# Optimization experiments

Measured on AMD Instinct MI355X. Metric: run time of the kernel, lower is better.

The kernel has to match this reference:

```python
import jax, jax.numpy as jnp
import numpy as np

N = 100000          # query / support points
H = 32              # neighbors per point
CIN = 32
COUT = 64
K = 15              # kernel points
KP_EXTENT = 1.0
KERNEL_RADIUS = KP_EXTENT * 1.5


def setup_inputs() -> dict:
    key = jax.random.key(0)
    k1, k2, k3, k4, k5, k6 = jax.random.split(key, 6)
    query = jax.random.uniform(k1, (N, 3), dtype=jnp.float32)
    support = jax.random.uniform(k2, (N, 3), dtype=jnp.float32)
    edge_indices = jax.random.randint(k3, (N, H), 0, N, dtype=jnp.int32)
    features = jax.random.normal(k4, (N, CIN), dtype=jnp.float32)
    # kernel point positions within kernel radius (fixed, non-trainable)
    K_points = jax.random.normal(k5, (K, 3), dtype=jnp.float32) * (KERNEL_RADIUS / 3.0)
    K_points = K_points.at[0].set(0.0)  # fixed='center'
    # xavier-normal kernel weights [K, CIN, COUT]
    std = jnp.sqrt(2.0 / (CIN + COUT)).astype(jnp.float32)
    K_values = jax.random.normal(k6, (K, CIN, COUT), dtype=jnp.float32) * std
    return {"query": query, "support": support, "edge_indices": edge_indices,
            "features": features, "K_points": K_points, "K_values": K_values}


def reference(query, support, edge_indices, features, K_points, K_values):
    # shadow point / shadow feature for out-of-range indices
    shadow_pt = jnp.ones_like(support[:1]) * 1e6
    support_ext = jnp.concatenate([support, shadow_pt], axis=0)      # [N+1, 3]
    feats_ext = jnp.concatenate([features, jnp.zeros_like(features[:1])], axis=0)  # [N+1, CIN]

    neighbors = support_ext[edge_indices] - query[:, None, :]        # [N, H, 3]
    # squared distances to each kernel point: [N, H, K]
    diff = neighbors[:, :, None, :] - K_points[None, None, :, :]     # [N, H, K, 3]
    sq_distances = jnp.sum(diff * diff, axis=-1)                     # [N, H, K]

    # linear influence, transposed to [N, K, H]
    all_weights = jnp.maximum(1.0 - jnp.sqrt(sq_distances) / KP_EXTENT, 0.0)
    all_weights = jnp.swapaxes(all_weights, 1, 2)                    # [N, K, H]

    # aggregation_mode == 'sum': no masking
    neighborhood_features = feats_ext[edge_indices]                  # [N, H, CIN]
    weighted = jnp.einsum('nkh,nhc->nkc', all_weights, neighborhood_features)  # [N, K, CIN]
    # per-kernel-point matmul then sum over kernel points
    out = jnp.einsum('nkc,kco->no', weighted, K_values)              # [N, COUT]
    return out
```

## Files before the change

### kernel.cpp

```cpp
#include <hip/hip_runtime.h>
#include <hip/hip_bf16.h>

typedef __attribute__((ext_vector_type(8))) short short8;
typedef __attribute__((ext_vector_type(4))) float f32x4;
typedef __attribute__((ext_vector_type(2))) unsigned int u32x2;

#define HH    32
#define CINN  32
#define COUTT 64
#define KNUM  15

static __device__ __forceinline__ short bfbits(float f) {
    __hip_bfloat16 h = __float2bfloat16(f);
    short s; __builtin_memcpy(&s, &h, 2); return s;
}
static __device__ __forceinline__ unsigned packbf(float a, float b) {
    return (unsigned)(unsigned short)bfbits(a) | ((unsigned)(unsigned short)bfbits(b) << 16);
}

static __device__ __forceinline__ void lds_barrier() {
    asm volatile("s_waitcnt lgkmcnt(0)" ::: "memory");
    __builtin_amdgcn_s_barrier();
    __builtin_amdgcn_sched_barrier(0);
}

__global__ void cvt_feats_kernel(const float* __restrict__ f,
                                 unsigned short* __restrict__ o, int n8) {
    int i = blockIdx.x * blockDim.x + threadIdx.x;
    if (i < n8) {
        f32x4 v0 = *(const f32x4*)(f + i * 8);
        f32x4 v1 = *(const f32x4*)(f + i * 8 + 4);
        u32x2 s0 = { packbf(v0.x, v0.y), packbf(v0.z, v0.w) };
        u32x2 s1 = { packbf(v1.x, v1.y), packbf(v1.z, v1.w) };
        *(u32x2*)(o + i * 8)     = s0;
        *(u32x2*)(o + i * 8 + 4) = s1;
    }
}

__launch_bounds__(256, 4)
__global__ void kpconv_kernel(const float* __restrict__ query,
                              const float* __restrict__ support,
                              const int*   __restrict__ edge,
                              const unsigned short* __restrict__ featsbf,
                              const float* __restrict__ kpts,
                              const float* __restrict__ kvals,
                              float* __restrict__ out,
                              int nPts, int nBatch) {
    __shared__ unsigned short af_lds[KNUM * 64 * 8];
    __shared__ f32x4 xyz[4][4][32];

    const int tid  = threadIdx.x;
    const int wave = tid >> 6;
    const int lane = tid & 63;
    const int g    = lane >> 4;
    const int low  = lane & 15;
    const int jpar = lane >> 5;
    const int l32  = lane & 31;
    const int slotA = ((l32 & 7) << 2) | (l32 >> 3);

    short8 kvreg[KNUM];
    #pragma unroll
    for (int s = 0; s < KNUM; ++s) {
        #pragma unroll
        for (int i = 0; i < 8; ++i) {
            int cp   = (g << 3) + i;
            int chan = (((cp & 15) << 1) | (cp >> 4));
            int o    = (wave << 4) + low;
            kvreg[s][i] = bfbits(kvals[(s * CINN + chan) * COUTT + o]);
        }
    }

    float px = 1e4f, py = 1e4f, pz = 1e4f;
    if (low < KNUM) { px = kpts[low * 3 + 0]; py = kpts[low * 3 + 1]; pz = kpts[low * 3 + 2]; }

    const int  ld0  = (wave << 2) + ((g >> 1) << 4);
    const int  half = (g & 1) << 3;
    const int  dM   = (low & 7) << 4;
    const int  T0   = (low * 64 + ld0) * 16 + half;
    const int  T1   = T0 + 32 * 16;
    const bool sact = (low < KNUM);
    const unsigned lbase = (unsigned)lane << 4;

    int   eN[2]; float sxN[2], syN[2], szN[2], qxN[2], qyN[2], qzN[2];
    #define LOADA(bb)                                                          \
        _Pragma("unroll")                                                      \
        for (int k = 0; k < 2; ++k) {                                          \
            int n = (bb) * 16 + (wave << 2) + (k << 1) + jpar;                 \
            if (n >= nPts) n = nPts - 1;                                       \
            int e = edge[n * HH + l32];                                        \
            eN[k] = e;                                                         \
            const float* qp = query + n * 3;                                   \
            const float* sp = support + (size_t)(unsigned)e * 3;               \
            sxN[k] = sp[0]; syN[k] = sp[1]; szN[k] = sp[2];                    \
            qxN[k] = qp[0]; qyN[k] = qp[1]; qzN[k] = qp[2];                    \
        }

    LOADA(blockIdx.x);

    __syncthreads();

    for (int b = blockIdx.x; b < nBatch; b += gridDim.x) {
        #pragma unroll
        for (int k = 0; k < 2; ++k) {
            f32x4 v = { sxN[k] - qxN[k], syN[k] - qyN[k], szN[k] - qzN[k],
                        __int_as_float(eN[k]) };
            xyz[wave][(k << 1) + jpar][slotA] = v;
        }

        LOADA(b + gridDim.x);

        #pragma unroll
        for (int p = 0; p < 4; ++p) {
            const f32x4* xrow = &xyz[wave][p][g];

            unsigned fd[8];
            short8 wf;
            #pragma unroll
            for (int i = 0; i < 8; ++i) {
                f32x4 v = xrow[i << 2];
                unsigned e = (unsigned)__float_as_int(v.w);
                fd[i] = *(const unsigned*)((const char*)featsbf + (e << 6) + ((unsigned)low << 2));
                float tx = v.x - px, ty = v.y - py, tz = v.z - pz;
                float d2 = fmaf(tx, tx, fmaf(ty, ty, tz * tz));
                wf[i] = bfbits(fmaxf(1.f - __builtin_amdgcn_sqrtf(d2), 0.f));
            }

            short8 a0, a1;
            #pragma unroll
            for (int i = 0; i < 8; ++i) {
                a0[i] = (short)(fd[i] & 0xffffu);
                a1[i] = (short)(fd[i] >> 16);
            }

            f32x4 c0 = {0.f, 0.f, 0.f, 0.f}, c1 = {0.f, 0.f, 0.f, 0.f};
            c0 = __builtin_amdgcn_mfma_f32_16x16x32_bf16(a0, wf, c0, 0, 0, 0);
            c1 = __builtin_amdgcn_mfma_f32_16x16x32_bf16(a1, wf, c1, 0, 0, 0);

            if (sact) {
                u32x2 w0 = { packbf(c0.x, c0.y), packbf(c0.z, c0.w) };
                u32x2 w1 = { packbf(c1.x, c1.y), packbf(c1.z, c1.w) };
                *(u32x2*)((char*)af_lds + ((T0 + (p << 4)) ^ dM)) = w0;
                *(u32x2*)((char*)af_lds + ((T1 + (p << 4)) ^ dM)) = w1;
            }
        }
        lds_barrier();

        f32x4 acc = {0.f, 0.f, 0.f, 0.f};
        #pragma unroll
        for (int s = 0; s < KNUM; ++s) {
            const char* ap = (const char*)af_lds + (lbase ^ (unsigned)((s & 7) << 4)) + s * 1024;
            short8 av = *(const short8*)ap;
            acc = __builtin_amdgcn_mfma_f32_16x16x32_bf16(av, kvreg[s], acc, 0, 0, 0);
        }

        {
            int n0 = b * 16 + (g << 2);
            float* orow = out + (size_t)(unsigned)n0 * COUTT + (wave << 4) + low;
            #pragma unroll
            for (int r = 0; r < 4; ++r) {
                if (n0 + r < nPts) orow[r * COUTT] = acc[r];
            }
        }
        lds_barrier();
    }
    #undef LOADA
}

extern "C" void kernel_launch(void* const* d_in, const int* in_sizes, int n_in,
                              void* d_out, int out_size, void* d_ws, size_t ws_size,
                              hipStream_t stream) {
    const float* query   = (const float*)d_in[0];
    const float* support = (const float*)d_in[1];
    const int*   edge    = (const int*)d_in[2];
    const float* feats   = (const float*)d_in[3];
    const float* kpts    = (const float*)d_in[4];
    const float* kvals   = (const float*)d_in[5];
    float* out = (float*)d_out;

    int nPts   = in_sizes[0] / 3;
    int nBatch = (nPts + 15) / 16;

    unsigned short* featsbf = (unsigned short*)d_ws;
    int n8 = nPts * CINN / 8;
    hipLaunchKernelGGL(cvt_feats_kernel, dim3((n8 + 255) / 256), dim3(256), 0, stream,
                       feats, featsbf, n8);

    int grid = 1536;
    if (grid > nBatch) grid = nBatch;

    hipLaunchKernelGGL(kpconv_kernel, dim3(grid), dim3(256), 0, stream,
                       query, support, edge, featsbf, kpts, kvals, out, nPts, nBatch);
}
```

Measured before the change: 161.6 us.

## Batch feature gathers across two rows and precompute squared norms

Edge indices move into a separate LDS array. Feature gathers for two neighbor rows are now issued together, before the weight computation, to raise memory-level parallelism. The squared distance is expanded as |x|^2 - 2x·p + |p|^2, with |x|^2 computed once per neighbor, which changes float rounding slightly. Kernel weights are packed to bf16 pairs in registers, occupancy is lowered to 3 waves per SIMD, and the grid is halved to 768 blocks. The extra gathered features in flight and the packed weights raise register pressure.

```diff
diff --git a/kernel.cpp b/kernel.cpp
--- a/kernel.cpp
+++ b/kernel.cpp
@@ -37,7 +37,7 @@
     }
 }
 
-__launch_bounds__(256, 4)
+__launch_bounds__(256, 3)
 __global__ void kpconv_kernel(const float* __restrict__ query,
                               const float* __restrict__ support,
                               const int*   __restrict__ edge,
@@ -48,6 +48,7 @@
                               int nPts, int nBatch) {
     __shared__ unsigned short af_lds[KNUM * 64 * 8];
     __shared__ f32x4 xyz[4][4][32];
+    __shared__ int   earr[4][4][32];
 
     const int tid  = threadIdx.x;
     const int wave = tid >> 6;
@@ -58,20 +59,26 @@
     const int l32  = lane & 31;
     const int slotA = ((l32 & 7) << 2) | (l32 >> 3);
 
-    short8 kvreg[KNUM];
+    unsigned kvu[KNUM][4];
     #pragma unroll
     for (int s = 0; s < KNUM; ++s) {
         #pragma unroll
-        for (int i = 0; i < 8; ++i) {
-            int cp   = (g << 3) + i;
-            int chan = (((cp & 15) << 1) | (cp >> 4));
-            int o    = (wave << 4) + low;
-            kvreg[s][i] = bfbits(kvals[(s * CINN + chan) * COUTT + o]);
-        }
+        for (int d = 0; d < 4; ++d) {
+            int cp0 = (g << 3) + 2 * d, cp1 = cp0 + 1;
+            int ch0 = ((cp0 & 15) << 1) | (cp0 >> 4);
+            int ch1 = ((cp1 & 15) << 1) | (cp1 >> 4);
+            int o   = (wave << 4) + low;
+            kvu[s][d] = packbf(kvals[(s * CINN + ch0) * COUTT + o],
+                               kvals[(s * CINN + ch1) * COUTT + o]);
+        }
+        asm volatile("" : "+v"(kvu[s][0]), "+v"(kvu[s][1]),
+                          "+v"(kvu[s][2]), "+v"(kvu[s][3]));
     }
 
     float px = 1e4f, py = 1e4f, pz = 1e4f;
     if (low < KNUM) { px = kpts[low * 3 + 0]; py = kpts[low * 3 + 1]; pz = kpts[low * 3 + 2]; }
+    const float m2px = -2.f * px, m2py = -2.f * py, m2pz = -2.f * pz;
+    const float ppsq = px * px + py * py + pz * pz;
 
     const int  ld0  = (wave << 2) + ((g >> 1) << 4);
     const int  half = (g & 1) << 3;
@@ -102,45 +109,53 @@
     for (int b = blockIdx.x; b < nBatch; b += gridDim.x) {
         #pragma unroll
         for (int k = 0; k < 2; ++k) {
-            f32x4 v = { sxN[k] - qxN[k], syN[k] - qyN[k], szN[k] - qzN[k],
-                        __int_as_float(eN[k]) };
-            xyz[wave][(k << 1) + jpar][slotA] = v;
+            float dx = sxN[k] - qxN[k], dy = syN[k] - qyN[k], dz = szN[k] - qzN[k];
+            float nn = fmaf(dx, dx, fmaf(dy, dy, dz * dz));
+            xyz[wave][(k << 1) + jpar][slotA]  = (f32x4){dx, dy, dz, nn};
+            earr[wave][(k << 1) + jpar][slotA] = eN[k];
         }
 
         LOADA(b + gridDim.x);
 
         #pragma unroll
-        for (int p = 0; p < 4; ++p) {
-            const f32x4* xrow = &xyz[wave][p][g];
-
-            unsigned fd[8];
-            short8 wf;
+        for (int pb = 0; pb < 4; pb += 2) {
+            unsigned fd[2][8];
             #pragma unroll
-            for (int i = 0; i < 8; ++i) {
-                f32x4 v = xrow[i << 2];
-                unsigned e = (unsigned)__float_as_int(v.w);
-                fd[i] = *(const unsigned*)((const char*)featsbf + (e << 6) + ((unsigned)low << 2));
-                float tx = v.x - px, ty = v.y - py, tz = v.z - pz;
-                float d2 = fmaf(tx, tx, fmaf(ty, ty, tz * tz));
-                wf[i] = bfbits(fmaxf(1.f - __builtin_amdgcn_sqrtf(d2), 0.f));
+            for (int q = 0; q < 2; ++q) {
+                #pragma unroll
+                for (int i = 0; i < 8; ++i) {
+                    unsigned e = (unsigned)earr[wave][pb + q][(i << 2) | g];
+                    fd[q][i] = *(const unsigned*)((const char*)featsbf +
+                                 (e << 6) + ((unsigned)low << 2));
+                }
             }
 
-            short8 a0, a1;
             #pragma unroll
-            for (int i = 0; i < 8; ++i) {
-                a0[i] = (short)(fd[i] & 0xffffu);
-                a1[i] = (short)(fd[i] >> 16);
-            }
-
-            f32x4 c0 = {0.f, 0.f, 0.f, 0.f}, c1 = {0.f, 0.f, 0.f, 0.f};
-            c0 = __builtin_amdgcn_mfma_f32_16x16x32_bf16(a0, wf, c0, 0, 0, 0);
-            c1 = __builtin_amdgcn_mfma_f32_16x16x32_bf16(a1, wf, c1, 0, 0, 0);
-
-            if (sact) {
-                u32x2 w0 = { packbf(c0.x, c0.y), packbf(c0.z, c0.w) };
-                u32x2 w1 = { packbf(c1.x, c1.y), packbf(c1.z, c1.w) };
-                *(u32x2*)((char*)af_lds + ((T0 + (p << 4)) ^ dM)) = w0;
-                *(u32x2*)((char*)af_lds + ((T1 + (p << 4)) ^ dM)) = w1;
+            for (int q = 0; q < 2; ++q) {
+                const int p = pb + q;
+                const f32x4* xrow = &xyz[wave][p][g];
+
+                short8 wf, a0, a1;
+                #pragma unroll
+                for (int i = 0; i < 8; ++i) {
+                    f32x4 v = xrow[i << 2];
+                    float d2 = fmaf(v.x, m2px, fmaf(v.y, m2py,
+                               fmaf(v.z, m2pz, v.w + ppsq)));
+                    wf[i] = bfbits(fmaxf(1.f - __builtin_amdgcn_sqrtf(d2), 0.f));
+                    a0[i] = (short)(fd[q][i] & 0xffffu);
+                    a1[i] = (short)(fd[q][i] >> 16);
+                }
+
+                f32x4 c0 = {0.f, 0.f, 0.f, 0.f}, c1 = {0.f, 0.f, 0.f, 0.f};
+                c0 = __builtin_amdgcn_mfma_f32_16x16x32_bf16(a0, wf, c0, 0, 0, 0);
+                c1 = __builtin_amdgcn_mfma_f32_16x16x32_bf16(a1, wf, c1, 0, 0, 0);
+
+                if (sact) {
+                    u32x2 w0 = { packbf(c0.x, c0.y), packbf(c0.z, c0.w) };
+                    u32x2 w1 = { packbf(c1.x, c1.y), packbf(c1.z, c1.w) };
+                    *(u32x2*)((char*)af_lds + ((T0 + (p << 4)) ^ dM)) = w0;
+                    *(u32x2*)((char*)af_lds + ((T1 + (p << 4)) ^ dM)) = w1;
+                }
             }
         }
         lds_barrier();
@@ -150,7 +165,8 @@
         for (int s = 0; s < KNUM; ++s) {
             const char* ap = (const char*)af_lds + (lbase ^ (unsigned)((s & 7) << 4)) + s * 1024;
             short8 av = *(const short8*)ap;
-            acc = __builtin_amdgcn_mfma_f32_16x16x32_bf16(av, kvreg[s], acc, 0, 0, 0);
+            short8 bv; __builtin_memcpy(&bv, kvu[s], 16);
+            acc = __builtin_amdgcn_mfma_f32_16x16x32_bf16(av, bv, acc, 0, 0, 0);
         }
 
         {
@@ -185,7 +201,7 @@
     hipLaunchKernelGGL(cvt_feats_kernel, dim3((n8 + 255) / 256), dim3(256), 0, stream,
                        feats, featsbf, n8);
 
-    int grid = 1536;
+    int grid = 768;
     if (grid > nBatch) grid = nBatch;
 
     hipLaunchKernelGGL(kpconv_kernel, dim3(grid), dim3(256), 0, stream,
```

Result: faster. 139.1 us (-13.9%).
